# Kernel tuning notes

Measured on AMD Instinct MI355X. Metric: run time of the kernel, lower is better.

## Reference

```python
import jax, jax.numpy as jnp
import numpy as np

K_GAUSS = 10
HIDDEN = 512


def setup_inputs() -> dict:
    key = jax.random.key(0)
    k1, k2, k3 = jax.random.split(key, 3)
    lstm_out = jax.random.normal(k1, (16, 1024, HIDDEN), dtype=jnp.float32)
    char_seq = jax.random.uniform(k2, (16, 600, 80), dtype=jnp.float32)
    # Dense(3*k_gaussians): small init so exp(params) stays in a sane range
    W = jax.random.normal(k3, (HIDDEN, 3 * K_GAUSS), dtype=jnp.float32) * 0.02
    bias = jnp.zeros((3 * K_GAUSS,), dtype=jnp.float32)
    return {"lstm_out": lstm_out, "char_seq": char_seq, "W": W, "bias": bias}


def reference(lstm_out, char_seq, W, bias):
    # lstm_out: [B,T,H], char_seq: [B,U,A]
    U = char_seq.shape[1]
    params = jnp.einsum('bth,hp->btp', lstm_out, W) + bias  # [B,T,3K]
    exp_params = jnp.exp(params)
    a, b, k = jnp.split(exp_params, 3, axis=2)              # each [B,T,K]
    u = jnp.arange(U, dtype=lstm_out.dtype).reshape(1, 1, U, 1)  # char indices
    # gaussian mixture window weights phi[b,t,u] = sum_k a*exp(-b*(k-u)^2)
    gaussians = a[:, :, None, :] * jnp.exp(-b[:, :, None, :] * jnp.square(k[:, :, None, :] - u))  # [B,T,U,K]
    char_weights = jnp.sum(gaussians, axis=3)               # [B,T,U]
    # alphabet_window[b,t,a] = sum_u phi[b,t,u] * char_seq[b,u,a]
    return jnp.einsum('btu,bua->bta', char_weights, char_seq)
```

## Files before the change

### kernel.cpp

```cpp
#include <hip/hip_runtime.h>
#include <math.h>

#define BB 16
#define TD 1024
#define HD 512
#define UD 600
#define AD 80
#define KG 10
#define PC 30
#define PP 32

#define LOG2E 1.4426950408889634f

#if __has_builtin(__builtin_amdgcn_exp2f)
#define EXP2F(x) __builtin_amdgcn_exp2f(x)
#else
#define EXP2F(x) exp2f(x)
#endif

typedef short v8s __attribute__((ext_vector_type(8)));
typedef float v4f __attribute__((ext_vector_type(4)));

__device__ inline unsigned short f2bf(float f) {
    unsigned u = __float_as_uint(f);
    return (unsigned short)((u + 0x7FFF + ((u >> 16) & 1)) >> 16);
}

__global__ void k_wprep(const float* __restrict__ W,
                        unsigned short* __restrict__ Wfh,
                        unsigned short* __restrict__ Wfl) {
    int p = blockIdx.x * 256 + threadIdx.x;
    for (; p < 32768; p += 256 * 32) {
        int j = p & 7, l = (p >> 3) & 63, n = (p >> 9) & 1, kt = p >> 10;
        int k = kt * 32 + ((l >> 4) * 8) + j;
        int c = n * 16 + (l & 15);
        float v = (c < PC) ? W[k * PC + c] : 0.f;
        unsigned short h = f2bf(v);
        float hi_f = __uint_as_float(((unsigned)h) << 16);
        Wfh[p] = h;
        Wfl[p] = f2bf(v - hi_f);
    }
}

__global__ __launch_bounds__(256) void k_params(const float* __restrict__ x,
                                                const unsigned short* __restrict__ Wfh,
                                                const unsigned short* __restrict__ Wfl,
                                                const float* __restrict__ bias,
                                                float* __restrict__ ep) {
    __shared__ float red[4 * 16 * 33];

    int tid = threadIdx.x;
    int wv = tid >> 6;
    int l = tid & 63;
    int quad = l >> 4, m = l & 15;
    long row0 = (long)blockIdx.x * 16;

    const float* xr = x + (row0 + m) * HD + wv * 128 + quad * 8;

    v4f acc[2] = {{0.f, 0.f, 0.f, 0.f}, {0.f, 0.f, 0.f, 0.f}};

    #pragma unroll
    for (int kt = 0; kt < 4; kt++) {
        float4 xa = *(const float4*)(xr + kt * 32);
        float4 xb = *(const float4*)(xr + kt * 32 + 4);
        float xf[8] = {xa.x, xa.y, xa.z, xa.w, xb.x, xb.y, xb.z, xb.w};
        v8s ah, al;
        #pragma unroll
        for (int j = 0; j < 8; j++) {
            unsigned short h = f2bf(xf[j]);
            ah[j] = (short)h;
            al[j] = (short)f2bf(xf[j] - __uint_as_float(((unsigned)h) << 16));
        }
        int ktg = wv * 4 + kt;
        #pragma unroll
        for (int n = 0; n < 2; n++) {
            uint4 uh = *(const uint4*)&Wfh[((ktg * 2 + n) * 64 + l) * 8];
            uint4 ul = *(const uint4*)&Wfl[((ktg * 2 + n) * 64 + l) * 8];
            v8s bh, bl;
            __builtin_memcpy(&bh, &uh, 16);
            __builtin_memcpy(&bl, &ul, 16);
            acc[n] = __builtin_amdgcn_mfma_f32_16x16x32_bf16(ah, bh, acc[n], 0, 0, 0);
            acc[n] = __builtin_amdgcn_mfma_f32_16x16x32_bf16(al, bh, acc[n], 0, 0, 0);
            acc[n] = __builtin_amdgcn_mfma_f32_16x16x32_bf16(ah, bl, acc[n], 0, 0, 0);
        }
    }

    #pragma unroll
    for (int n = 0; n < 2; n++)
        #pragma unroll
        for (int r = 0; r < 4; r++)
            red[wv * 528 + (quad * 4 + r) * 33 + n * 16 + m] = acc[n][r];
    __syncthreads();

    for (int idx = tid; idx < 16 * PP; idx += 256) {
        int mm = idx >> 5, c = idx & 31;
        float val = 0.f;
        if (c < PC) {
            float s = red[0 * 528 + mm * 33 + c] + red[1 * 528 + mm * 33 + c]
                    + red[2 * 528 + mm * 33 + c] + red[3 * 528 + mm * 33 + c];
            float e = __expf(s + bias[c]);
            val = (c >= 10 && c < 20) ? (-e * LOG2E) : e;
        }
        ep[(row0 + mm) * PP + c] = val;
    }
}

#define TT 32
#define UC 40
#define NCHUNK 15
#define NTHR 320

__global__ __launch_bounds__(NTHR) void k_main(const float* __restrict__ ep,
                                               const float* __restrict__ cs,
                                               float* __restrict__ out) {
    __shared__ float params_l[TT * 36];
    __shared__ float cs_l[UC * AD];
    __shared__ float phi2[TT * 44];
    __shared__ float range_l[2];

    int tid = threadIdx.x;
    int b = blockIdx.y;
    int t0 = blockIdx.x * TT;
    long r0 = (long)b * TD + t0;

    if (tid < 256) {
        float4 v = *(const float4*)(ep + r0 * PP + tid * 4);
        int tt_ = tid >> 3, j = (tid & 7) * 4;
        *(float4*)&params_l[tt_ * 36 + j] = v;
    }
    __syncthreads();

    int tt = tid & 31;
    int sub = tid >> 5;
    float pa[KG], pnb[KG], pk[KG];
    #pragma unroll
    for (int q = 0; q < KG; q++) {
        pa[q]  = params_l[tt * 36 + q];
        pnb[q] = params_l[tt * 36 + 10 + q];
        pk[q]  = params_l[tt * 36 + 20 + q];
    }

    {
        float lo = 1e30f, hi = -1e30f;
        #pragma unroll
        for (int q = 0; q < KG; q++) {
            float bits = 46.f + fmaxf(0.f, __log2f(pa[q]));
            float w = __fsqrt_rn(bits / (-pnb[q]));
            lo = fminf(lo, pk[q] - w);
            hi = fmaxf(hi, pk[q] + w);
        }
        if (tid < 64) {
            #pragma unroll
            for (int mk = 1; mk < 64; mk <<= 1) {
                lo = fminf(lo, __shfl_xor(lo, mk));
                hi = fmaxf(hi, __shfl_xor(hi, mk));
            }
            if (tid == 0) { range_l[0] = lo; range_l[1] = hi; }
        }
    }
    __syncthreads();
    float lo_m = fminf(fmaxf(range_l[0], 0.f), (float)(UD - 1));
    float hi_m = fminf(fmaxf(range_l[1], 0.f), (float)(UD - 1));
    int ch_lo = (int)lo_m / UC;
    int ch_hi = (int)hi_m / UC;
    if (ch_lo > ch_hi) ch_lo = ch_hi;

    int tx = tid % 20;
    int ty = tid / 20;
    float4 acc0 = {0.f, 0.f, 0.f, 0.f};
    float4 acc1 = {0.f, 0.f, 0.f, 0.f};

    const float* csb = cs + (long)b * UD * AD;

    for (int ch = ch_lo; ch <= ch_hi; ch++) {
        int u0 = ch * UC;
        __syncthreads();

        for (int idx = tid; idx < (UC * AD) / 4; idx += NTHR) {
            *(float4*)&cs_l[idx * 4] = *(const float4*)&csb[u0 * AD + idx * 4];
        }

        float ph[4];
        #pragma unroll
        for (int i = 0; i < 4; i++) {
            float uf = (float)(u0 + sub * 4 + i);
            float ss = 0.f;
            #pragma unroll
            for (int q = 0; q < KG; q++) {
                float d = uf - pk[q];
                ss += pa[q] * EXP2F(pnb[q] * d * d);
            }
            ph[i] = ss;
        }
        *(float4*)&phi2[tt * 44 + sub * 4] = make_float4(ph[0], ph[1], ph[2], ph[3]);
        __syncthreads();

        #pragma unroll 2
        for (int g = 0; g < 10; g++) {
            float4 p0 = *(const float4*)&phi2[(ty * 2) * 44 + g * 4];
            float4 p1 = *(const float4*)&phi2[(ty * 2 + 1) * 44 + g * 4];
            #pragma unroll
            for (int i = 0; i < 4; i++) {
                float4 c4 = *(const float4*)&cs_l[(g * 4 + i) * AD + tx * 4];
                float pi0 = (i == 0) ? p0.x : (i == 1) ? p0.y : (i == 2) ? p0.z : p0.w;
                float pi1 = (i == 0) ? p1.x : (i == 1) ? p1.y : (i == 2) ? p1.z : p1.w;
                acc0.x += pi0 * c4.x; acc0.y += pi0 * c4.y;
                acc0.z += pi0 * c4.z; acc0.w += pi0 * c4.w;
                acc1.x += pi1 * c4.x; acc1.y += pi1 * c4.y;
                acc1.z += pi1 * c4.z; acc1.w += pi1 * c4.w;
            }
        }
    }

    long t = r0 + ty * 2;
    *(float4*)(out + t * AD + tx * 4) = acc0;
    *(float4*)(out + (t + 1) * AD + tx * 4) = acc1;
}

extern "C" void kernel_launch(void* const* d_in, const int* in_sizes, int n_in,
                              void* d_out, int out_size, void* d_ws, size_t ws_size,
                              hipStream_t stream) {
    const float* lstm = (const float*)d_in[0];
    const float* cs   = (const float*)d_in[1];
    const float* W    = (const float*)d_in[2];
    const float* bias = (const float*)d_in[3];
    float* out = (float*)d_out;

    float* ep = (float*)d_ws;
    unsigned short* Wfh = (unsigned short*)((char*)d_ws + (16384L * PP * 4));
    unsigned short* Wfl = Wfh + 32768;

    k_wprep<<<32, 256, 0, stream>>>(W, Wfh, Wfl);
    k_params<<<(BB * TD) / 16, 256, 0, stream>>>(lstm, Wfh, Wfl, bias, ep);
    dim3 grid(TD / TT, BB);
    k_main<<<grid, NTHR, 0, stream>>>(ep, cs, out);
}
```

Measured before the change: 93.00 us.

## Fuse projection GEMM into main window kernel, dropping params workspace

Removes the separate params kernel and computes the 32-row projection via bf16-split MFMA inside the main kernel, writing exp'd params straight to shared memory. This eliminates one launch and the global write/read of the intermediate params buffer. In exchange, each main block now serially loads its slice of lstm_out before the window computation, and only four of five waves participate in the GEMM, with larger shared memory use.

```diff
diff --git a/kernel.cpp b/kernel.cpp
--- a/kernel.cpp
+++ b/kernel.cpp
@@ -42,77 +42,18 @@
     }
 }
 
-__global__ __launch_bounds__(256) void k_params(const float* __restrict__ x,
-                                                const unsigned short* __restrict__ Wfh,
-                                                const unsigned short* __restrict__ Wfl,
-                                                const float* __restrict__ bias,
-                                                float* __restrict__ ep) {
-    __shared__ float red[4 * 16 * 33];
-
-    int tid = threadIdx.x;
-    int wv = tid >> 6;
-    int l = tid & 63;
-    int quad = l >> 4, m = l & 15;
-    long row0 = (long)blockIdx.x * 16;
-
-    const float* xr = x + (row0 + m) * HD + wv * 128 + quad * 8;
-
-    v4f acc[2] = {{0.f, 0.f, 0.f, 0.f}, {0.f, 0.f, 0.f, 0.f}};
-
-    #pragma unroll
-    for (int kt = 0; kt < 4; kt++) {
-        float4 xa = *(const float4*)(xr + kt * 32);
-        float4 xb = *(const float4*)(xr + kt * 32 + 4);
-        float xf[8] = {xa.x, xa.y, xa.z, xa.w, xb.x, xb.y, xb.z, xb.w};
-        v8s ah, al;
-        #pragma unroll
-        for (int j = 0; j < 8; j++) {
-            unsigned short h = f2bf(xf[j]);
-            ah[j] = (short)h;
-            al[j] = (short)f2bf(xf[j] - __uint_as_float(((unsigned)h) << 16));
-        }
-        int ktg = wv * 4 + kt;
-        #pragma unroll
-        for (int n = 0; n < 2; n++) {
-            uint4 uh = *(const uint4*)&Wfh[((ktg * 2 + n) * 64 + l) * 8];
-            uint4 ul = *(const uint4*)&Wfl[((ktg * 2 + n) * 64 + l) * 8];
-            v8s bh, bl;
-            __builtin_memcpy(&bh, &uh, 16);
-            __builtin_memcpy(&bl, &ul, 16);
-            acc[n] = __builtin_amdgcn_mfma_f32_16x16x32_bf16(ah, bh, acc[n], 0, 0, 0);
-            acc[n] = __builtin_amdgcn_mfma_f32_16x16x32_bf16(al, bh, acc[n], 0, 0, 0);
-            acc[n] = __builtin_amdgcn_mfma_f32_16x16x32_bf16(ah, bl, acc[n], 0, 0, 0);
-        }
-    }
-
-    #pragma unroll
-    for (int n = 0; n < 2; n++)
-        #pragma unroll
-        for (int r = 0; r < 4; r++)
-            red[wv * 528 + (quad * 4 + r) * 33 + n * 16 + m] = acc[n][r];
-    __syncthreads();
-
-    for (int idx = tid; idx < 16 * PP; idx += 256) {
-        int mm = idx >> 5, c = idx & 31;
-        float val = 0.f;
-        if (c < PC) {
-            float s = red[0 * 528 + mm * 33 + c] + red[1 * 528 + mm * 33 + c]
-                    + red[2 * 528 + mm * 33 + c] + red[3 * 528 + mm * 33 + c];
-            float e = __expf(s + bias[c]);
-            val = (c >= 10 && c < 20) ? (-e * LOG2E) : e;
-        }
-        ep[(row0 + mm) * PP + c] = val;
-    }
-}
-
 #define TT 32
 #define UC 40
 #define NCHUNK 15
 #define NTHR 320
 
-__global__ __launch_bounds__(NTHR) void k_main(const float* __restrict__ ep,
-                                               const float* __restrict__ cs,
-                                               float* __restrict__ out) {
+__global__ __launch_bounds__(NTHR) void k_fused(const float* __restrict__ x,
+                                                const unsigned short* __restrict__ Wfh,
+                                                const unsigned short* __restrict__ Wfl,
+                                                const float* __restrict__ bias,
+                                                const float* __restrict__ cs,
+                                                float* __restrict__ out) {
+    __shared__ float red[4 * TT * 33];
     __shared__ float params_l[TT * 36];
     __shared__ float cs_l[UC * AD];
     __shared__ float phi2[TT * 44];
@@ -123,10 +64,68 @@
     int t0 = blockIdx.x * TT;
     long r0 = (long)b * TD + t0;
 
-    if (tid < 256) {
-        float4 v = *(const float4*)(ep + r0 * PP + tid * 4);
-        int tt_ = tid >> 3, j = (tid & 7) * 4;
-        *(float4*)&params_l[tt_ * 36 + j] = v;
+    int wv = tid >> 6;
+    int l = tid & 63;
+    int quad = l >> 4, m = l & 15;
+
+    if (wv < 4) {
+        v4f acc[2][2];
+        #pragma unroll
+        for (int mt = 0; mt < 2; mt++)
+            #pragma unroll
+            for (int n = 0; n < 2; n++)
+                acc[mt][n] = (v4f){0.f, 0.f, 0.f, 0.f};
+
+        #pragma unroll
+        for (int kt = 0; kt < 4; kt++) {
+            int g = wv * 4 + kt;
+            v8s ah[2], al[2];
+            #pragma unroll
+            for (int mt = 0; mt < 2; mt++) {
+                const float* xr = x + (r0 + mt * 16 + m) * HD + g * 32 + quad * 8;
+                float4 xa = *(const float4*)(xr);
+                float4 xb = *(const float4*)(xr + 4);
+                float xf[8] = {xa.x, xa.y, xa.z, xa.w, xb.x, xb.y, xb.z, xb.w};
+                #pragma unroll
+                for (int j = 0; j < 8; j++) {
+                    unsigned short h = f2bf(xf[j]);
+                    ah[mt][j] = (short)h;
+                    al[mt][j] = (short)f2bf(xf[j] - __uint_as_float(((unsigned)h) << 16));
+                }
+            }
+            #pragma unroll
+            for (int n = 0; n < 2; n++) {
+                uint4 uh = *(const uint4*)&Wfh[((g * 2 + n) * 64 + l) * 8];
+                uint4 ul = *(const uint4*)&Wfl[((g * 2 + n) * 64 + l) * 8];
+                v8s bh, bl;
+                __builtin_memcpy(&bh, &uh, 16);
+                __builtin_memcpy(&bl, &ul, 16);
+                #pragma unroll
+                for (int mt = 0; mt < 2; mt++) {
+                    acc[mt][n] = __builtin_amdgcn_mfma_f32_16x16x32_bf16(ah[mt], bh, acc[mt][n], 0, 0, 0);
+                    acc[mt][n] = __builtin_amdgcn_mfma_f32_16x16x32_bf16(al[mt], bh, acc[mt][n], 0, 0, 0);
+                    acc[mt][n] = __builtin_amdgcn_mfma_f32_16x16x32_bf16(ah[mt], bl, acc[mt][n], 0, 0, 0);
+                }
+            }
+        }
+
+        #pragma unroll
+        for (int mt = 0; mt < 2; mt++)
+            #pragma unroll
+            for (int n = 0; n < 2; n++)
+                #pragma unroll
+                for (int r = 0; r < 4; r++)
+                    red[wv * (TT * 33) + (mt * 16 + quad * 4 + r) * 33 + n * 16 + m]
+                        = acc[mt][n][r];
+    }
+    __syncthreads();
+
+    for (int idx = tid; idx < TT * PC; idx += NTHR) {
+        int r = idx / PC, c = idx - r * PC;
+        float s = red[0 * (TT * 33) + r * 33 + c] + red[1 * (TT * 33) + r * 33 + c]
+                + red[2 * (TT * 33) + r * 33 + c] + red[3 * (TT * 33) + r * 33 + c];
+        float e = __expf(s + bias[c]);
+        params_l[r * 36 + c] = (c >= 10 && c < 20) ? (-e * LOG2E) : e;
     }
     __syncthreads();
 
@@ -226,12 +225,10 @@
     const float* bias = (const float*)d_in[3];
     float* out = (float*)d_out;
 
-    float* ep = (float*)d_ws;
-    unsigned short* Wfh = (unsigned short*)((char*)d_ws + (16384L * PP * 4));
+    unsigned short* Wfh = (unsigned short*)d_ws;
     unsigned short* Wfl = Wfh + 32768;
 
     k_wprep<<<32, 256, 0, stream>>>(W, Wfh, Wfl);
-    k_params<<<(BB * TD) / 16, 256, 0, stream>>>(lstm, Wfh, Wfl, bias, ep);
     dim3 grid(TD / TT, BB);
-    k_main<<<grid, NTHR, 0, stream>>>(ep, cs, out);
-}
+    k_fused<<<grid, NTHR, 0, stream>>>(lstm, Wfh, Wfl, bias, cs, out);
+}
```

New measurement: 89.10 us. 1.04x faster.
